# Kernel tuning notes

Measured on AMD Instinct MI355X. Metric: run time of the kernel, lower is better.

The kernel has to match this reference:

```python
import jax, jax.numpy as jnp
import numpy as np

N = 50000      # nodes
E = 800000     # edges (avg degree 16)
C = 5000       # clusters (Kongming compression)
D = 128        # in_features
OUT = 40       # out_features (classes)
K = 2          # propagation hops


def setup_inputs() -> dict:
    key = jax.random.key(0)
    k1, k2, k3, k4, k5, k6 = jax.random.split(key, 6)
    x = jax.random.normal(k1, (N, D), dtype=jnp.float32)
    edge_index = jax.random.randint(k2, (2, E), 0, N, dtype=jnp.int32)
    cluster_index = jax.random.randint(k3, (N,), 0, C, dtype=jnp.int32)
    rep_idx = jax.random.randint(k4, (C,), 0, N, dtype=jnp.int32)
    W = jax.random.normal(k5, (OUT, D), dtype=jnp.float32) / np.sqrt(D)
    b = jax.random.normal(k6, (OUT,), dtype=jnp.float32) * 0.01
    return {"x": x, "edge_index": edge_index, "cluster_index": cluster_index,
            "rep_idx": rep_idx, "W": W, "b": b}


def _gcn_propagate(x, edge_index, k_hops):
    # PUPropagate: K hops of D^{-1/2}(A+I)D^{-1/2} x (gcn_norm with self-loops)
    n = x.shape[0]
    loops = jnp.arange(n, dtype=edge_index.dtype)
    src = jnp.concatenate([edge_index[0], loops])
    dst = jnp.concatenate([edge_index[1], loops])
    deg = jax.ops.segment_sum(jnp.ones_like(src, dtype=x.dtype), dst, num_segments=n)
    dinv = jnp.where(deg > 0, jax.lax.rsqrt(deg), 0.0)
    norm = (dinv[src] * dinv[dst])[:, None]            # [E+N, 1]
    h = x
    for _ in range(k_hops):                            # small fixed hop count
        h = jax.ops.segment_sum(h[src] * norm, dst, num_segments=n)
    return h


def reference(x, edge_index, cluster_index, rep_idx, W, b):
    h = _gcn_propagate(x, edge_index, K)               # [N, D]
    # Kongming_Cluster: gather one representative row per cluster
    hc = h[rep_idx]                                    # [C, D]
    yc = hc @ W.T + b                                  # [C, OUT] dense linear on compressed rows
    # Kongming_Reconstruct: scatter back to all nodes by cluster index
    y = yc[cluster_index]                              # [N, OUT]
    return jax.nn.log_softmax(y, axis=1)
```

## Files before the change

kernel.cpp:

```cpp
#include <hip/hip_runtime.h>
#include <math.h>

#define N_NODES 50000
#define N_EDGES 800000
#define N_CLUST 5000
#define DIM     128
#define NOUT    40
#define SLOTS   64
#define CSLOT   64

#define FILL_PART   4
#define NODES_PER_P (N_NODES / FILL_PART)
#define FILL_CHUNKS 250
#define EI4         (N_EDGES / 4)
#define CI4         (EI4 / FILL_CHUNKS)

#define ZB2    391
#define INVB   50
#define FILLB  1000
#define GRID_A (ZB2 + INVB + FILLB)

typedef __attribute__((ext_vector_type(8))) short short8;
typedef __attribute__((ext_vector_type(4))) float fvec4;
typedef __attribute__((ext_vector_type(4))) int ivec4;

__device__ __forceinline__ short bf16r(float v) {
    unsigned u = __float_as_uint(v);
    u = (u + 0x7FFFu + ((u >> 16) & 1u)) >> 16;
    return (short)u;
}
__device__ __forceinline__ unsigned pack_bf16x2(float a, float b) {
    unsigned ua = __float_as_uint(a);
    unsigned ub = __float_as_uint(b);
    ua = (ua + 0x7FFFu + ((ua >> 16) & 1u)) >> 16;
    ub = (ub + 0x7FFFu + ((ub >> 16) & 1u)) >> 16;
    return ua | (ub << 16);
}
__device__ __forceinline__ float2 unpack_bf16x2(unsigned v) {
    float2 r;
    r.x = __uint_as_float(v << 16);
    r.y = __uint_as_float(v & 0xFFFF0000u);
    return r;
}
__device__ __forceinline__ float4 unpack_bf16x4(uint2 v) {
    float4 r;
    r.x = __uint_as_float(v.x << 16);
    r.y = __uint_as_float(v.x & 0xFFFF0000u);
    r.z = __uint_as_float(v.y << 16);
    r.w = __uint_as_float(v.y & 0xFFFF0000u);
    return r;
}

__global__ __launch_bounds__(256) void fused_A(const float* __restrict__ x,
                                               const int* __restrict__ esrc,
                                               const int* __restrict__ edst,
                                               const int* __restrict__ cidx,
                                               const float* __restrict__ W,
                                               int* __restrict__ cnt,
                                               int* __restrict__ ccnt,
                                               unsigned short* __restrict__ slot,
                                               unsigned short* __restrict__ zs,
                                               unsigned short* __restrict__ cinv) {
    int lane = threadIdx.x & 63;
    int wv = threadIdx.x >> 6;

    if (blockIdx.x < ZB2) {
        int gw = blockIdx.x * 4 + wv;
        int q = lane >> 4, r16 = lane & 15;

        short8 bfr[3][4];
        #pragma unroll
        for (int t = 0; t < 3; t++) {
            int o = t * 16 + r16;
            #pragma unroll
            for (int s = 0; s < 4; s++) {
                short8 f = {0, 0, 0, 0, 0, 0, 0, 0};
                if (o < NOUT) {
                    const float* wp = W + o * DIM + s * 32 + q * 8;
                    float4 w0 = *(const float4*)wp;
                    float4 w1 = *(const float4*)(wp + 4);
                    f[0] = bf16r(w0.x); f[1] = bf16r(w0.y);
                    f[2] = bf16r(w0.z); f[3] = bf16r(w0.w);
                    f[4] = bf16r(w1.x); f[5] = bf16r(w1.y);
                    f[6] = bf16r(w1.z); f[7] = bf16r(w1.w);
                }
                bfr[t][s] = f;
            }
        }

        for (int tile = gw; tile < N_NODES / 16; tile += ZB2 * 4) {
            int node = tile * 16 + r16;
            short8 af[4];
            #pragma unroll
            for (int s = 0; s < 4; s++) {
                const fvec4* xp = (const fvec4*)(x + (size_t)node * DIM + s * 32 + q * 8);
                fvec4 a0 = __builtin_nontemporal_load(xp);
                fvec4 a1 = __builtin_nontemporal_load(xp + 1);
                short8 f;
                f[0] = bf16r(a0.x); f[1] = bf16r(a0.y);
                f[2] = bf16r(a0.z); f[3] = bf16r(a0.w);
                f[4] = bf16r(a1.x); f[5] = bf16r(a1.y);
                f[6] = bf16r(a1.z); f[7] = bf16r(a1.w);
                af[s] = f;
            }

            fvec4 acc0 = {0, 0, 0, 0}, acc1 = {0, 0, 0, 0}, acc2 = {0, 0, 0, 0};
            #pragma unroll
            for (int s = 0; s < 4; s++) {
                acc0 = __builtin_amdgcn_mfma_f32_16x16x32_bf16(af[s], bfr[0][s], acc0, 0, 0, 0);
                acc1 = __builtin_amdgcn_mfma_f32_16x16x32_bf16(af[s], bfr[1][s], acc1, 0, 0, 0);
                acc2 = __builtin_amdgcn_mfma_f32_16x16x32_bf16(af[s], bfr[2][s], acc2, 0, 0, 0);
            }

            #pragma unroll
            for (int r = 0; r < 4; r++) {
                int nd = tile * 16 + q * 4 + r;
                unsigned short* zrow = zs + (size_t)nd * NOUT;
                __builtin_nontemporal_store((unsigned short)bf16r(acc0[r]), &zrow[r16]);
                __builtin_nontemporal_store((unsigned short)bf16r(acc1[r]), &zrow[16 + r16]);
                if (r16 < 8)
                    __builtin_nontemporal_store((unsigned short)bf16r(acc2[r]), &zrow[32 + r16]);
            }
        }
    } else if (blockIdx.x < ZB2 + INVB) {
        int t0 = (blockIdx.x - ZB2) * 256 + threadIdx.x;
        for (int i = t0; i < N_NODES; i += INVB * 256) {
            int c = cidx[i];
            int pos = atomicAdd(&ccnt[c], 1);
            if (pos < CSLOT) cinv[c * CSLOT + pos] = (unsigned short)i;
        }
    } else {
        int fb = blockIdx.x - ZB2 - INVB;
        const ivec4* src4 = (const ivec4*)esrc;
        const ivec4* dst4 = (const ivec4*)edst;
        int p = fb & (FILL_PART - 1);
        int chunk = fb >> 2;
        int lo = p * NODES_PER_P;
        int hi = lo + NODES_PER_P;
        int q0 = chunk * CI4;
        for (int i = threadIdx.x; i < CI4; i += 256) {
            ivec4 d4 = __builtin_nontemporal_load(&dst4[q0 + i]);
            ivec4 s4 = __builtin_nontemporal_load(&src4[q0 + i]);
            if (d4.x >= lo && d4.x < hi) {
                int pos = atomicAdd(&cnt[d4.x], 1);
                if (pos < SLOTS) slot[d4.x * SLOTS + pos] = (unsigned short)s4.x;
            }
            if (d4.y >= lo && d4.y < hi) {
                int pos = atomicAdd(&cnt[d4.y], 1);
                if (pos < SLOTS) slot[d4.y * SLOTS + pos] = (unsigned short)s4.y;
            }
            if (d4.z >= lo && d4.z < hi) {
                int pos = atomicAdd(&cnt[d4.z], 1);
                if (pos < SLOTS) slot[d4.z * SLOTS + pos] = (unsigned short)s4.z;
            }
            if (d4.w >= lo && d4.w < hi) {
                int pos = atomicAdd(&cnt[d4.w], 1);
                if (pos < SLOTS) slot[d4.w * SLOTS + pos] = (unsigned short)s4.w;
            }
        }
    }
}

__global__ __launch_bounds__(256) void scale_zd(const uint2* __restrict__ zs2,
                                                uint2* __restrict__ zd2,
                                                const int* __restrict__ cnt) {
    int i = blockIdx.x * 256 + threadIdx.x;
    if (i >= N_NODES * 10) return;
    int n = i / 10;
    float dn = rsqrtf((float)(cnt[n] + 1));
    float4 f = unpack_bf16x4(zs2[i]);
    uint2 p;
    p.x = pack_bf16x2(dn * f.x, dn * f.y);
    p.y = pack_bf16x2(dn * f.z, dn * f.w);
    zd2[i] = p;
}

__global__ __launch_bounds__(256) void hop_all(const uint2* __restrict__ zd2,
                                               uint2* __restrict__ v12,
                                               const unsigned short* __restrict__ slot,
                                               const int* __restrict__ cnt) {
    int lane = threadIdx.x & 63;
    int g = lane / 10;
    int k = lane - g * 10;
    int wv = threadIdx.x >> 6;
    int n = blockIdx.x * 24 + wv * 6 + g;
    if (g >= 6 || n >= N_NODES) return;
    int c = cnt[n];
    int m = (c < SLOTS) ? c : SLOTS;
    float s = 1.0f / (float)(c + 1);
    float4 accA = unpack_bf16x4(zd2[n * 10 + k]);
    float4 accB; accB.x = accB.y = accB.z = accB.w = 0.0f;
    int base = n * SLOTS;
    int j = 0;
    for (; j + 7 < m; j += 8) {
        unsigned ss0 = *(const unsigned*)&slot[base + j];
        unsigned ss1 = *(const unsigned*)&slot[base + j + 2];
        unsigned ss2 = *(const unsigned*)&slot[base + j + 4];
        unsigned ss3 = *(const unsigned*)&slot[base + j + 6];
        float4 f0 = unpack_bf16x4(zd2[(int)(ss0 & 0xFFFFu) * 10 + k]);
        float4 f1 = unpack_bf16x4(zd2[(int)(ss0 >> 16) * 10 + k]);
        float4 f2 = unpack_bf16x4(zd2[(int)(ss1 & 0xFFFFu) * 10 + k]);
        float4 f3 = unpack_bf16x4(zd2[(int)(ss1 >> 16) * 10 + k]);
        float4 f4 = unpack_bf16x4(zd2[(int)(ss2 & 0xFFFFu) * 10 + k]);
        float4 f5 = unpack_bf16x4(zd2[(int)(ss2 >> 16) * 10 + k]);
        float4 f6 = unpack_bf16x4(zd2[(int)(ss3 & 0xFFFFu) * 10 + k]);
        float4 f7 = unpack_bf16x4(zd2[(int)(ss3 >> 16) * 10 + k]);
        accA.x += (f0.x + f1.x) + (f4.x + f5.x);
        accA.y += (f0.y + f1.y) + (f4.y + f5.y);
        accA.z += (f0.z + f1.z) + (f4.z + f5.z);
        accA.w += (f0.w + f1.w) + (f4.w + f5.w);
        accB.x += (f2.x + f3.x) + (f6.x + f7.x);
        accB.y += (f2.y + f3.y) + (f6.y + f7.y);
        accB.z += (f2.z + f3.z) + (f6.z + f7.z);
        accB.w += (f2.w + f3.w) + (f6.w + f7.w);
    }
    for (; j + 1 < m; j += 2) {
        unsigned ss0 = *(const unsigned*)&slot[base + j];
        float4 f0 = unpack_bf16x4(zd2[(int)(ss0 & 0xFFFFu) * 10 + k]);
        float4 f1 = unpack_bf16x4(zd2[(int)(ss0 >> 16) * 10 + k]);
        accA.x += f0.x + f1.x;  accA.y += f0.y + f1.y;
        accA.z += f0.z + f1.z;  accA.w += f0.w + f1.w;
    }
    if (j < m) {
        float4 f0 = unpack_bf16x4(zd2[(int)slot[base + j] * 10 + k]);
        accB.x += f0.x; accB.y += f0.y; accB.z += f0.z; accB.w += f0.w;
    }
    uint2 p;
    p.x = pack_bf16x2(s * (accA.x + accB.x), s * (accA.y + accB.y));
    p.y = pack_bf16x2(s * (accA.z + accB.z), s * (accA.w + accB.w));
    v12[n * 10 + k] = p;
}

__global__ __launch_bounds__(256) void rep_scatter(const unsigned* __restrict__ v1,
                                                   const unsigned short* __restrict__ slot,
                                                   const int* __restrict__ cnt,
                                                   const int* __restrict__ ccnt,
                                                   const unsigned short* __restrict__ cinv,
                                                   const int* __restrict__ rep_idx,
                                                   const float2* __restrict__ b2,
                                                   float2* __restrict__ out2) {
    int lane = threadIdx.x & 63;
    int wv = threadIdx.x >> 6;
    int c = blockIdx.x * 4 + wv;
    if (c >= N_CLUST) return;
    int n = rep_idx[c];
    int cn = cnt[n];
    int m = (cn < SLOTS) ? cn : SLOTS;
    float dn = rsqrtf((float)(cn + 1));
    int g = lane / 20;
    int k = lane - g * 20;
    float2 acc; acc.x = 0.0f; acc.y = 0.0f;
    if (g == 0) acc = unpack_bf16x2(v1[n * 20 + k]);
    if (g < 3) {
        int base = n * SLOTS;
        for (int j = g; j < m; j += 3) {
            float2 f = unpack_bf16x2(v1[(int)slot[base + j] * 20 + k]);
            acc.x += f.x; acc.y += f.y;
        }
    }
    float t1x = __shfl(acc.x, lane + 20), t1y = __shfl(acc.y, lane + 20);
    float t2x = __shfl(acc.x, lane + 40), t2y = __shfl(acc.y, lane + 40);
    bool act = (lane < 20);
    float2 h; h.x = 0.0f; h.y = 0.0f;
    if (act) {
        float2 bb = b2[k];
        h.x = dn * (acc.x + t1x + t2x) + bb.x;
        h.y = dn * (acc.y + t1y + t2y) + bb.y;
    }
    float mx = act ? fmaxf(h.x, h.y) : -INFINITY;
    #pragma unroll
    for (int off = 32; off; off >>= 1) mx = fmaxf(mx, __shfl_xor(mx, off));
    float e = act ? (expf(h.x - mx) + expf(h.y - mx)) : 0.0f;
    #pragma unroll
    for (int off = 32; off; off >>= 1) e += __shfl_xor(e, off);
    float lg = mx + logf(e);
    float2 o; o.x = h.x - lg; o.y = h.y - lg;
    int mc = ccnt[c];
    if (mc > CSLOT) mc = CSLOT;
    const unsigned short* mem = cinv + c * CSLOT;
    for (int idx = 0; idx < mc; idx++) {
        int node = (int)mem[idx];
        if (act) out2[(size_t)node * 20 + k] = o;
    }
}

extern "C" void kernel_launch(void* const* d_in, const int* in_sizes, int n_in,
                              void* d_out, int out_size, void* d_ws, size_t ws_size,
                              hipStream_t stream) {
    const float* x    = (const float*)d_in[0];
    const int*   esrc = (const int*)d_in[1];
    const int*   edst = ((const int*)d_in[1]) + N_EDGES;
    const int*   cidx = (const int*)d_in[2];
    const int*   ridx = (const int*)d_in[3];
    const float* W    = (const float*)d_in[4];
    const float* b    = (const float*)d_in[5];
    float* out = (float*)d_out;

    char* ws = (char*)d_ws;
    size_t off = 0;
    auto alloc = [&](size_t bytes) { char* p = ws + off; off += (bytes + 255) & ~size_t(255); return p; };
    int*            cnt  = (int*)alloc((N_NODES + N_CLUST) * 4);
    int*            ccnt = cnt + N_NODES;
    unsigned short* slot = (unsigned short*)alloc((size_t)N_NODES * SLOTS * 2);
    unsigned short* zs   = (unsigned short*)alloc((size_t)N_NODES * NOUT * 2);
    unsigned short* zd   = (unsigned short*)alloc((size_t)N_NODES * NOUT * 2);
    unsigned*       v1   = (unsigned*)alloc((size_t)N_NODES * (NOUT / 2) * 4);
    unsigned short* cinv = (unsigned short*)alloc((size_t)N_CLUST * CSLOT * 2);
    (void)ws_size; (void)in_sizes; (void)n_in; (void)out_size;

    hipMemsetAsync(cnt, 0, (N_NODES + N_CLUST) * 4, stream);

    fused_A<<<GRID_A, 256, 0, stream>>>(x, esrc, edst, cidx, W,
                                        cnt, ccnt, slot, zs, cinv);
    scale_zd<<<(N_NODES * 10 + 255) / 256, 256, 0, stream>>>((const uint2*)zs,
                                                             (uint2*)zd, cnt);
    hop_all<<<(N_NODES + 23) / 24, 256, 0, stream>>>((const uint2*)zd, (uint2*)v1,
                                                     slot, cnt);
    rep_scatter<<<(N_CLUST + 3) / 4, 256, 0, stream>>>((const unsigned*)v1, slot, cnt,
                                                       ccnt, cinv, ridx,
                                                       (const float2*)b, (float2*)out);
}
```

Measured before the change: 157.8 us.

## Replace global-atomic adjacency fill with two-level bucketed binning via shared memory

The edge fill no longer does a per-edge global atomic into per-node counters. Each block now bins its edges into 391 buckets of 128 destination nodes using shared-memory atomics, reserves space with one global atomic per bucket, and writes packed (dst,src) pairs. A new build_scale kernel then builds per-node slot lists with shared atomics and applies the degree scaling, replacing the separate scale_zd pass. The projection section now has each wave handle exactly one 16-node tile and uses plain loads. The goal is to cut global atomic contention and the redundant edge-partition rereads, at the cost of an extra bucket buffer that overflows past a fixed cap of 2560 entries.

```diff
diff --git a/kernel.cpp b/kernel.cpp
--- a/kernel.cpp
+++ b/kernel.cpp
@@ -9,16 +9,15 @@
 #define SLOTS   64
 #define CSLOT   64
 
-#define FILL_PART   4
-#define NODES_PER_P (N_NODES / FILL_PART)
-#define FILL_CHUNKS 250
-#define EI4         (N_EDGES / 4)
-#define CI4         (EI4 / FILL_CHUNKS)
-
-#define ZB2    391
+#define NBKT    391
+#define BCAP    2560
+#define GB_STR  16
+#define BUCKB   250
+#define EPB4    800
+
+#define ZB     782
 #define INVB   50
-#define FILLB  1000
-#define GRID_A (ZB2 + INVB + FILLB)
+#define GRID_A (ZB + INVB + BUCKB)
 
 typedef __attribute__((ext_vector_type(8))) short short8;
 typedef __attribute__((ext_vector_type(4))) float fvec4;
@@ -56,16 +55,19 @@
                                                const int* __restrict__ edst,
                                                const int* __restrict__ cidx,
                                                const float* __restrict__ W,
-                                               int* __restrict__ cnt,
                                                int* __restrict__ ccnt,
-                                               unsigned short* __restrict__ slot,
                                                unsigned short* __restrict__ zs,
-                                               unsigned short* __restrict__ cinv) {
+                                               unsigned short* __restrict__ cinv,
+                                               int* __restrict__ gbcnt,
+                                               unsigned* __restrict__ gbuck) {
+    __shared__ int bcnt[NBKT];
+    __shared__ int bbase[NBKT];
     int lane = threadIdx.x & 63;
     int wv = threadIdx.x >> 6;
 
-    if (blockIdx.x < ZB2) {
+    if (blockIdx.x < ZB) {
         int gw = blockIdx.x * 4 + wv;
+        if (gw >= N_NODES / 16) return;
         int q = lane >> 4, r16 = lane & 15;
 
         short8 bfr[3][4];
@@ -88,91 +90,138 @@
             }
         }
 
-        for (int tile = gw; tile < N_NODES / 16; tile += ZB2 * 4) {
-            int node = tile * 16 + r16;
-            short8 af[4];
-            #pragma unroll
-            for (int s = 0; s < 4; s++) {
-                const fvec4* xp = (const fvec4*)(x + (size_t)node * DIM + s * 32 + q * 8);
-                fvec4 a0 = __builtin_nontemporal_load(xp);
-                fvec4 a1 = __builtin_nontemporal_load(xp + 1);
-                short8 f;
-                f[0] = bf16r(a0.x); f[1] = bf16r(a0.y);
-                f[2] = bf16r(a0.z); f[3] = bf16r(a0.w);
-                f[4] = bf16r(a1.x); f[5] = bf16r(a1.y);
-                f[6] = bf16r(a1.z); f[7] = bf16r(a1.w);
-                af[s] = f;
-            }
-
-            fvec4 acc0 = {0, 0, 0, 0}, acc1 = {0, 0, 0, 0}, acc2 = {0, 0, 0, 0};
-            #pragma unroll
-            for (int s = 0; s < 4; s++) {
-                acc0 = __builtin_amdgcn_mfma_f32_16x16x32_bf16(af[s], bfr[0][s], acc0, 0, 0, 0);
-                acc1 = __builtin_amdgcn_mfma_f32_16x16x32_bf16(af[s], bfr[1][s], acc1, 0, 0, 0);
-                acc2 = __builtin_amdgcn_mfma_f32_16x16x32_bf16(af[s], bfr[2][s], acc2, 0, 0, 0);
-            }
-
-            #pragma unroll
-            for (int r = 0; r < 4; r++) {
-                int nd = tile * 16 + q * 4 + r;
-                unsigned short* zrow = zs + (size_t)nd * NOUT;
-                __builtin_nontemporal_store((unsigned short)bf16r(acc0[r]), &zrow[r16]);
-                __builtin_nontemporal_store((unsigned short)bf16r(acc1[r]), &zrow[16 + r16]);
-                if (r16 < 8)
-                    __builtin_nontemporal_store((unsigned short)bf16r(acc2[r]), &zrow[32 + r16]);
-            }
-        }
-    } else if (blockIdx.x < ZB2 + INVB) {
-        int t0 = (blockIdx.x - ZB2) * 256 + threadIdx.x;
+        int tile = gw;
+        int node = tile * 16 + r16;
+        short8 af[4];
+        #pragma unroll
+        for (int s = 0; s < 4; s++) {
+            const fvec4* xp = (const fvec4*)(x + (size_t)node * DIM + s * 32 + q * 8);
+            fvec4 a0 = *xp;
+            fvec4 a1 = *(xp + 1);
+            short8 f;
+            f[0] = bf16r(a0.x); f[1] = bf16r(a0.y);
+            f[2] = bf16r(a0.z); f[3] = bf16r(a0.w);
+            f[4] = bf16r(a1.x); f[5] = bf16r(a1.y);
+            f[6] = bf16r(a1.z); f[7] = bf16r(a1.w);
+            af[s] = f;
+        }
+
+        fvec4 acc0 = {0, 0, 0, 0}, acc1 = {0, 0, 0, 0}, acc2 = {0, 0, 0, 0};
+        #pragma unroll
+        for (int s = 0; s < 4; s++) {
+            acc0 = __builtin_amdgcn_mfma_f32_16x16x32_bf16(af[s], bfr[0][s], acc0, 0, 0, 0);
+            acc1 = __builtin_amdgcn_mfma_f32_16x16x32_bf16(af[s], bfr[1][s], acc1, 0, 0, 0);
+            acc2 = __builtin_amdgcn_mfma_f32_16x16x32_bf16(af[s], bfr[2][s], acc2, 0, 0, 0);
+        }
+
+        #pragma unroll
+        for (int r = 0; r < 4; r++) {
+            int nd = tile * 16 + q * 4 + r;
+            unsigned short* zrow = zs + (size_t)nd * NOUT;
+            __builtin_nontemporal_store((unsigned short)bf16r(acc0[r]), &zrow[r16]);
+            __builtin_nontemporal_store((unsigned short)bf16r(acc1[r]), &zrow[16 + r16]);
+            if (r16 < 8)
+                __builtin_nontemporal_store((unsigned short)bf16r(acc2[r]), &zrow[32 + r16]);
+        }
+    } else if (blockIdx.x < ZB + INVB) {
+        int t0 = (blockIdx.x - ZB) * 256 + threadIdx.x;
         for (int i = t0; i < N_NODES; i += INVB * 256) {
             int c = cidx[i];
             int pos = atomicAdd(&ccnt[c], 1);
             if (pos < CSLOT) cinv[c * CSLOT + pos] = (unsigned short)i;
         }
     } else {
-        int fb = blockIdx.x - ZB2 - INVB;
+        int fb = blockIdx.x - ZB - INVB;
         const ivec4* src4 = (const ivec4*)esrc;
         const ivec4* dst4 = (const ivec4*)edst;
-        int p = fb & (FILL_PART - 1);
-        int chunk = fb >> 2;
-        int lo = p * NODES_PER_P;
-        int hi = lo + NODES_PER_P;
-        int q0 = chunk * CI4;
-        for (int i = threadIdx.x; i < CI4; i += 256) {
-            ivec4 d4 = __builtin_nontemporal_load(&dst4[q0 + i]);
-            ivec4 s4 = __builtin_nontemporal_load(&src4[q0 + i]);
-            if (d4.x >= lo && d4.x < hi) {
-                int pos = atomicAdd(&cnt[d4.x], 1);
-                if (pos < SLOTS) slot[d4.x * SLOTS + pos] = (unsigned short)s4.x;
-            }
-            if (d4.y >= lo && d4.y < hi) {
-                int pos = atomicAdd(&cnt[d4.y], 1);
-                if (pos < SLOTS) slot[d4.y * SLOTS + pos] = (unsigned short)s4.y;
-            }
-            if (d4.z >= lo && d4.z < hi) {
-                int pos = atomicAdd(&cnt[d4.z], 1);
-                if (pos < SLOTS) slot[d4.z * SLOTS + pos] = (unsigned short)s4.z;
-            }
-            if (d4.w >= lo && d4.w < hi) {
-                int pos = atomicAdd(&cnt[d4.w], 1);
-                if (pos < SLOTS) slot[d4.w * SLOTS + pos] = (unsigned short)s4.w;
-            }
-        }
-    }
-}
-
-__global__ __launch_bounds__(256) void scale_zd(const uint2* __restrict__ zs2,
-                                                uint2* __restrict__ zd2,
-                                                const int* __restrict__ cnt) {
-    int i = blockIdx.x * 256 + threadIdx.x;
-    if (i >= N_NODES * 10) return;
-    int n = i / 10;
-    float dn = rsqrtf((float)(cnt[n] + 1));
-    float4 f = unpack_bf16x4(zs2[i]);
-    uint2 p;
-    p.x = pack_bf16x2(dn * f.x, dn * f.y);
-    p.y = pack_bf16x2(dn * f.z, dn * f.w);
-    zd2[i] = p;
+        int q0 = fb * EPB4;
+
+        for (int i = threadIdx.x; i < NBKT; i += 256) bcnt[i] = 0;
+        __syncthreads();
+
+        for (int i = threadIdx.x; i < EPB4; i += 256) {
+            ivec4 d4 = dst4[q0 + i];
+            atomicAdd(&bcnt[d4.x >> 7], 1);
+            atomicAdd(&bcnt[d4.y >> 7], 1);
+            atomicAdd(&bcnt[d4.z >> 7], 1);
+            atomicAdd(&bcnt[d4.w >> 7], 1);
+        }
+        __syncthreads();
+
+        for (int bk = threadIdx.x; bk < NBKT; bk += 256) {
+            int c = bcnt[bk];
+            bbase[bk] = c ? atomicAdd(&gbcnt[bk * GB_STR], c) : 0;
+        }
+        __syncthreads();
+        for (int i = threadIdx.x; i < NBKT; i += 256) bcnt[i] = 0;
+        __syncthreads();
+
+        for (int i = threadIdx.x; i < EPB4; i += 256) {
+            ivec4 d4 = dst4[q0 + i];
+            ivec4 s4 = src4[q0 + i];
+            {
+                int bk = d4.x >> 7; int idx = atomicAdd(&bcnt[bk], 1);
+                unsigned p = (unsigned)(bbase[bk] + idx);
+                if (p < BCAP) gbuck[(size_t)bk * BCAP + p] = ((unsigned)d4.x << 16) | (unsigned)s4.x;
+            }
+            {
+                int bk = d4.y >> 7; int idx = atomicAdd(&bcnt[bk], 1);
+                unsigned p = (unsigned)(bbase[bk] + idx);
+                if (p < BCAP) gbuck[(size_t)bk * BCAP + p] = ((unsigned)d4.y << 16) | (unsigned)s4.y;
+            }
+            {
+                int bk = d4.z >> 7; int idx = atomicAdd(&bcnt[bk], 1);
+                unsigned p = (unsigned)(bbase[bk] + idx);
+                if (p < BCAP) gbuck[(size_t)bk * BCAP + p] = ((unsigned)d4.z << 16) | (unsigned)s4.z;
+            }
+            {
+                int bk = d4.w >> 7; int idx = atomicAdd(&bcnt[bk], 1);
+                unsigned p = (unsigned)(bbase[bk] + idx);
+                if (p < BCAP) gbuck[(size_t)bk * BCAP + p] = ((unsigned)d4.w << 16) | (unsigned)s4.w;
+            }
+        }
+    }
+}
+
+__global__ __launch_bounds__(256) void build_scale(const unsigned* __restrict__ gbuck,
+                                                   const int* __restrict__ gbcnt,
+                                                   const uint2* __restrict__ zs2,
+                                                   int* __restrict__ cnt,
+                                                   unsigned short* __restrict__ slot,
+                                                   uint2* __restrict__ zd2) {
+    __shared__ int c128[128];
+    int b = blockIdx.x;
+    if (threadIdx.x < 128) c128[threadIdx.x] = 0;
+    __syncthreads();
+    int m = gbcnt[b * GB_STR];
+    if (m > BCAP) m = BCAP;
+    const unsigned* bk = gbuck + (size_t)b * BCAP;
+    for (int i = threadIdx.x; i < m; i += 256) {
+        unsigned e = bk[i];
+        int d7 = (int)(e >> 16) & 127;
+        int pos = atomicAdd(&c128[d7], 1);
+        if (pos < SLOTS)
+            slot[((size_t)((b << 7) + d7)) * SLOTS + pos] = (unsigned short)(e & 0xFFFFu);
+    }
+    __syncthreads();
+    int n0 = b << 7;
+    if (threadIdx.x < 128) {
+        int n = n0 + threadIdx.x;
+        if (n < N_NODES) cnt[n] = c128[threadIdx.x];
+    }
+    for (int i = threadIdx.x; i < 128 * 10; i += 256) {
+        int r = i / 10;
+        int n = n0 + r;
+        if (n < N_NODES) {
+            int k = i - r * 10;
+            float dn = rsqrtf((float)(c128[r] + 1));
+            float4 f = unpack_bf16x4(zs2[(size_t)n * 10 + k]);
+            uint2 p;
+            p.x = pack_bf16x2(dn * f.x, dn * f.y);
+            p.y = pack_bf16x2(dn * f.z, dn * f.w);
+            zd2[(size_t)n * 10 + k] = p;
+        }
+    }
 }
 
 __global__ __launch_bounds__(256) void hop_all(const uint2* __restrict__ zd2,
@@ -299,21 +348,23 @@
     char* ws = (char*)d_ws;
     size_t off = 0;
     auto alloc = [&](size_t bytes) { char* p = ws + off; off += (bytes + 255) & ~size_t(255); return p; };
-    int*            cnt  = (int*)alloc((N_NODES + N_CLUST) * 4);
-    int*            ccnt = cnt + N_NODES;
-    unsigned short* slot = (unsigned short*)alloc((size_t)N_NODES * SLOTS * 2);
-    unsigned short* zs   = (unsigned short*)alloc((size_t)N_NODES * NOUT * 2);
-    unsigned short* zd   = (unsigned short*)alloc((size_t)N_NODES * NOUT * 2);
-    unsigned*       v1   = (unsigned*)alloc((size_t)N_NODES * (NOUT / 2) * 4);
-    unsigned short* cinv = (unsigned short*)alloc((size_t)N_CLUST * CSLOT * 2);
+    int*            cnt   = (int*)alloc((N_NODES + N_CLUST + NBKT * GB_STR) * 4);
+    int*            ccnt  = cnt + N_NODES;
+    int*            gbcnt = ccnt + N_CLUST;
+    unsigned short* slot  = (unsigned short*)alloc((size_t)N_NODES * SLOTS * 2);
+    unsigned short* zs    = (unsigned short*)alloc((size_t)N_NODES * NOUT * 2);
+    unsigned short* zd    = (unsigned short*)alloc((size_t)N_NODES * NOUT * 2);
+    unsigned*       v1    = (unsigned*)alloc((size_t)N_NODES * (NOUT / 2) * 4);
+    unsigned short* cinv  = (unsigned short*)alloc((size_t)N_CLUST * CSLOT * 2);
+    unsigned*       gbuck = (unsigned*)alloc((size_t)NBKT * BCAP * 4);
     (void)ws_size; (void)in_sizes; (void)n_in; (void)out_size;
 
-    hipMemsetAsync(cnt, 0, (N_NODES + N_CLUST) * 4, stream);
+    hipMemsetAsync(ccnt, 0, (N_CLUST + NBKT * GB_STR) * 4, stream);
 
     fused_A<<<GRID_A, 256, 0, stream>>>(x, esrc, edst, cidx, W,
-                                        cnt, ccnt, slot, zs, cinv);
-    scale_zd<<<(N_NODES * 10 + 255) / 256, 256, 0, stream>>>((const uint2*)zs,
-                                                             (uint2*)zd, cnt);
+                                        ccnt, zs, cinv, gbcnt, gbuck);
+    build_scale<<<NBKT, 256, 0, stream>>>(gbuck, gbcnt, (const uint2*)zs,
+                                          cnt, slot, (uint2*)zd);
     hop_all<<<(N_NODES + 23) / 24, 256, 0, stream>>>((const uint2*)zd, (uint2*)v1,
                                                      slot, cnt);
     rep_scatter<<<(N_CLUST + 3) / 4, 256, 0, stream>>>((const unsigned*)v1, slot, cnt,
```

Measured after the change: 141.4 us. 10.4% less time.
